# Kernel optimization log

Hardware: AMD Instinct MI355X
Metric: run time of the kernel (lower is better)

The kernel has to match this reference:

```python
import jax, jax.numpy as jnp
import numpy as np

FDIM, HDIM, DIM = 512, 512, 256
B, N = 64, 4096


def setup_inputs() -> dict:
    key = jax.random.key(0)
    k1, k2, k3, k4, k5 = jax.random.split(key, 5)
    image_features = jax.random.normal(k1, (B, N, FDIM), dtype=jnp.float32)
    hidden_state = jax.random.normal(k2, (B, HDIM), dtype=jnp.float32)
    # nn.Linear weights: stored [out, in]; y = x @ W.T
    W_img = jax.random.normal(k3, (DIM, FDIM), dtype=jnp.float32) * (FDIM ** -0.5)
    W_hid = jax.random.normal(k4, (DIM, HDIM), dtype=jnp.float32) * (HDIM ** -0.5)
    W_score = jax.random.normal(k5, (1, DIM), dtype=jnp.float32) * (DIM ** -0.5)
    return {"image_features": image_features, "hidden_state": hidden_state,
            "W_img": W_img, "W_hid": W_hid, "W_score": W_score}


def reference(image_features, hidden_state, W_img, W_hid, W_score):
    # proj_image: [B, N, D]
    proj_image = jnp.einsum('bnf,df->bnd', image_features, W_img)
    # proj_hidden: [B, 1, D]
    proj_hidden = jnp.einsum('bh,dh->bd', hidden_state, W_hid)[:, None, :]
    combined = jnp.tanh(proj_image + proj_hidden)            # [B, N, D]
    scores = jnp.einsum('bnd,d->bn', combined, W_score[0])   # [B, N]
    weights = jax.nn.softmax(scores, axis=-1)                # [B, N]
    context = jnp.einsum('bn,bnf->bf', weights, image_features)  # [B, F]
    return (context, weights)
```

## Files before the change

### kernel.cpp

```cpp
#include <hip/hip_runtime.h>
#include <hip/hip_bf16.h>

#define B_ 64
#define N_ 4096
#define F_ 512
#define D_ 256
#define BM 64
#define BK 64
#define APAD 520

typedef __attribute__((ext_vector_type(8))) short short8;
typedef __attribute__((ext_vector_type(4))) float f32x4;

__device__ __forceinline__ unsigned short f2bf(float f) {
  unsigned int u = __float_as_uint(f);
  u += 0x7FFFu + ((u >> 16) & 1u);
  return (unsigned short)(u >> 16);
}

__device__ __forceinline__ float fast_tanh(float x) {
  float e = __expf(-2.0f * fabsf(x));
  float t = (1.0f - e) / (1.0f + e);
  return copysignf(t, x);
}

__global__ void prep_w_kernel(const float* __restrict__ Wimg,
                              unsigned short* __restrict__ wfrag) {
  int d = blockIdx.x;
  int f = threadIdx.x;
  int kt = f >> 6, ks = (f >> 5) & 1, lg = (f >> 3) & 3, e = f & 7;
  int lr = d & 15, d16 = d >> 4;
  int lane = lg * 16 + lr;
  int idx = (((kt * 2 + ks) * 16 + d16) * 64 + lane) * 8 + e;
  wfrag[idx] = f2bf(Wimg[d * F_ + f]);
}

__global__ void prep_ph_kernel(const float* __restrict__ hid,
                               const float* __restrict__ Whid,
                               float* __restrict__ ph) {
  int b = blockIdx.x, d = threadIdx.x;
  const float4* hv = (const float4*)(hid + b * F_);
  const float4* wv = (const float4*)(Whid + d * F_);
  float acc = 0.f;
#pragma unroll 4
  for (int i = 0; i < 128; i++) {
    float4 h = hv[i], w = wv[i];
    acc += h.x * w.x + h.y * w.y + h.z * w.z + h.w * w.w;
  }
  ph[b * D_ + d] = acc;
}

__global__ __launch_bounds__(256, 2) void fused_kernel(
    const float* __restrict__ feat, const unsigned short* __restrict__ wfrag,
    const float* __restrict__ ph, const float* __restrict__ wscore,
    float* __restrict__ expw, float2* __restrict__ meta,
    float* __restrict__ part) {
  __shared__ unsigned short Afull[BM * APAD];
  __shared__ float red[BM][4];
  __shared__ float sbuf[BM];
  __shared__ float ewf[BM];

  int tid = threadIdx.x;
  int lane = tid & 63, wn = tid >> 6;
  int lr = lane & 15, lg = lane >> 4;

  int blk = blockIdx.x;
  int b = blk >> 6, chunk = blk & 63;
  int n0 = chunk * BM;

  const float* arow = feat + (size_t)(b * N_ + n0) * F_;

  f32x4 acc[4][4];
#pragma unroll
  for (int m = 0; m < 4; m++)
#pragma unroll
    for (int n = 0; n < 4; n++) acc[m][n] = (f32x4)0.f;

  int r_[4], c4_[4];
#pragma unroll
  for (int i = 0; i < 4; i++) {
    int idx4 = tid + i * 256;
    r_[i] = idx4 >> 4;
    c4_[i] = idx4 & 15;
  }

  float4 av[4];
#pragma unroll
  for (int i = 0; i < 4; i++)
    av[i] = *(const float4*)(arow + (size_t)r_[i] * F_ + c4_[i] * 4);
#pragma unroll
  for (int i = 0; i < 4; i++) {
    unsigned int p0 = (unsigned)f2bf(av[i].x) | ((unsigned)f2bf(av[i].y) << 16);
    unsigned int p1 = (unsigned)f2bf(av[i].z) | ((unsigned)f2bf(av[i].w) << 16);
    *(uint2*)(Afull + r_[i] * APAD + c4_[i] * 4) = make_uint2(p0, p1);
  }
  __syncthreads();

  for (int kt = 0; kt < F_ / BK; kt++) {
    if (kt < 7) {
#pragma unroll
      for (int i = 0; i < 4; i++)
        av[i] = *(const float4*)(arow + (size_t)r_[i] * F_ + (kt + 1) * BK + c4_[i] * 4);
    }
    short8 bfr[2][4], af[2][4];
#pragma unroll
    for (int ks = 0; ks < 2; ks++)
#pragma unroll
      for (int n = 0; n < 4; n++)
        bfr[ks][n] = *(const short8*)(wfrag +
            (size_t)(((kt * 2 + ks) * 16 + wn * 4 + n) * 64 + lane) * 8);
#pragma unroll
    for (int ks = 0; ks < 2; ks++)
#pragma unroll
      for (int m = 0; m < 4; m++)
        af[ks][m] = *(const short8*)(Afull + (m * 16 + lr) * APAD + kt * BK + ks * 32 + lg * 8);
#pragma unroll
    for (int ks = 0; ks < 2; ks++)
#pragma unroll
      for (int m = 0; m < 4; m++)
#pragma unroll
        for (int n = 0; n < 4; n++)
          acc[m][n] = __builtin_amdgcn_mfma_f32_16x16x32_bf16(af[ks][m], bfr[ks][n], acc[m][n], 0, 0, 0);
    if (kt < 7) {
#pragma unroll
      for (int i = 0; i < 4; i++) {
        unsigned int p0 = (unsigned)f2bf(av[i].x) | ((unsigned)f2bf(av[i].y) << 16);
        unsigned int p1 = (unsigned)f2bf(av[i].z) | ((unsigned)f2bf(av[i].w) << 16);
        *(uint2*)(Afull + r_[i] * APAD + (kt + 1) * BK + c4_[i] * 4) = make_uint2(p0, p1);
      }
    }
    __syncthreads();
  }

  float ph4[4], wv4[4];
#pragma unroll
  for (int n = 0; n < 4; n++) {
    int d = wn * 64 + n * 16 + lr;
    ph4[n] = ph[b * D_ + d];
    wv4[n] = wscore[d];
  }
#pragma unroll
  for (int m = 0; m < 4; m++) {
#pragma unroll
    for (int j = 0; j < 4; j++) {
      float p = 0.f;
#pragma unroll
      for (int n = 0; n < 4; n++)
        p += fast_tanh(acc[m][n][j] + ph4[n]) * wv4[n];
      p += __shfl_xor(p, 1);
      p += __shfl_xor(p, 2);
      p += __shfl_xor(p, 4);
      p += __shfl_xor(p, 8);
      if (lr == 0) red[m * 16 + lg * 4 + j][wn] = p;
    }
  }
  __syncthreads();
  if (tid < BM) sbuf[tid] = red[tid][0] + red[tid][1] + red[tid][2] + red[tid][3];
  __syncthreads();

  float mb = -1e30f;
#pragma unroll
  for (int r = 0; r < BM; r++) mb = fmaxf(mb, sbuf[r]);
  if (tid < BM) {
    float e = __expf(sbuf[tid] - mb);
    ewf[tid] = e;
    expw[b * N_ + n0 + tid] = e;
    float l = e;
#pragma unroll
    for (int o = 1; o < 64; o <<= 1) l += __shfl_xor(l, o);
    if (tid == 0) meta[blk] = make_float2(mb, l);
  }
  __syncthreads();

  int f0 = tid * 2;
  float a0 = 0.f, a1 = 0.f;
#pragma unroll 8
  for (int r = 0; r < BM; r++) {
    float w = ewf[r];
    unsigned int v = *(const unsigned int*)(Afull + r * APAD + f0);
    a0 += w * __uint_as_float(v << 16);
    a1 += w * __uint_as_float(v & 0xffff0000u);
  }
  float2 o; o.x = a0; o.y = a1;
  *(float2*)(part + (size_t)blk * F_ + f0) = o;
}

__global__ void finalize_kernel(const float* __restrict__ part,
                                const float2* __restrict__ meta,
                                const float* __restrict__ expw,
                                float* __restrict__ ctx,
                                float* __restrict__ wout) {
  __shared__ float sm[64], sl[64], se[64];
  int b = blockIdx.x, t = threadIdx.x;
  if (t < 64) {
    float2 ml = meta[b * 64 + t];
    sm[t] = ml.x;
    sl[t] = ml.y;
  }
  __syncthreads();
  float M = -1e30f;
#pragma unroll
  for (int i = 0; i < 64; i++) M = fmaxf(M, sm[i]);
  float Z = 0.f;
#pragma unroll
  for (int i = 0; i < 64; i++) Z += sl[i] * __expf(sm[i] - M);
  if (t < 64) se[t] = __expf(sm[t] - M);
  __syncthreads();
  float invZ = 1.0f / Z;
  float acc = 0.f;
#pragma unroll 8
  for (int i = 0; i < 64; i++) acc += part[(size_t)(b * 64 + i) * F_ + t] * se[i];
  ctx[b * F_ + t] = acc * invZ;
#pragma unroll
  for (int k = 0; k < 8; k++) {
    int n = k * 512 + t;
    wout[b * N_ + n] = expw[b * N_ + n] * se[n >> 6] * invZ;
  }
}

extern "C" void kernel_launch(void* const* d_in, const int* in_sizes, int n_in,
                              void* d_out, int out_size, void* d_ws, size_t ws_size,
                              hipStream_t stream) {
  const float* feat   = (const float*)d_in[0];
  const float* hid    = (const float*)d_in[1];
  const float* Wimg   = (const float*)d_in[2];
  const float* Whid   = (const float*)d_in[3];
  const float* Wscore = (const float*)d_in[4];

  float* ctx  = (float*)d_out;
  float* wout = (float*)d_out + B_ * F_;

  unsigned short* wfrag = (unsigned short*)d_ws;
  float*  ph    = (float*)((char*)d_ws + 262144);
  float*  expw  = (float*)((char*)d_ws + 327680);
  float2* meta  = (float2*)((char*)d_ws + 1376256);
  float*  part  = (float*)((char*)d_ws + 1409024);

  prep_w_kernel<<<D_, F_, 0, stream>>>(Wimg, wfrag);
  prep_ph_kernel<<<B_, D_, 0, stream>>>(hid, Whid, ph);
  fused_kernel<<<(B_ * N_) / BM, 256, 0, stream>>>(feat, wfrag, ph, Wscore, expw, meta, part);
  finalize_kernel<<<B_, 512, 0, stream>>>(part, meta, expw, ctx, wout);
}
```

Before: 241.3 us.

## Halve row tile, raise occupancy, and double-buffer feature prefetch across K steps

Shrinks the per-block row tile from 64 to 32 rows, which halves the shared-memory tile and allows four blocks per CU instead of two. The chunk count per batch row doubles, and the finalize kernel and workspace offsets are adjusted to match. The K loop now keeps two register buffers of feature loads in flight, and float-to-bf16 packing uses the packed intrinsic. The aim is to hide global-load latency on this memory-bound fused pass. In exchange, each block reloads the weight fragments for half as many rows, so weight traffic through the cache doubles, and the partial-context workspace and finalize reduction also double.

New measurement: 212.8 us. 11.8% less time.

```diff
diff --git a/kernel.cpp b/kernel.cpp
--- a/kernel.cpp
+++ b/kernel.cpp
@@ -5,9 +5,11 @@
 #define N_ 4096
 #define F_ 512
 #define D_ 256
-#define BM 64
+#define BM 32
 #define BK 64
 #define APAD 520
+#define NCHUNK (N_ / BM)
+#define NBLK (B_ * NCHUNK)
 
 typedef __attribute__((ext_vector_type(8))) short short8;
 typedef __attribute__((ext_vector_type(4))) float f32x4;
@@ -16,6 +18,13 @@
   unsigned int u = __float_as_uint(f);
   u += 0x7FFFu + ((u >> 16) & 1u);
   return (unsigned short)(u >> 16);
+}
+
+__device__ __forceinline__ unsigned int pk2bf(float x, float y) {
+  float2 f; f.x = x; f.y = y;
+  __hip_bfloat162 h = __float22bfloat162_rn(f);
+  union { __hip_bfloat162 h2; unsigned int u; } cv; cv.h2 = h;
+  return cv.u;
 }
 
 __device__ __forceinline__ float fast_tanh(float x) {
@@ -50,7 +59,7 @@
   ph[b * D_ + d] = acc;
 }
 
-__global__ __launch_bounds__(256, 2) void fused_kernel(
+__global__ __launch_bounds__(256, 4) void fused_kernel(
     const float* __restrict__ feat, const unsigned short* __restrict__ wfrag,
     const float* __restrict__ ph, const float* __restrict__ wscore,
     float* __restrict__ expw, float2* __restrict__ meta,
@@ -65,70 +74,64 @@
   int lr = lane & 15, lg = lane >> 4;
 
   int blk = blockIdx.x;
-  int b = blk >> 6, chunk = blk & 63;
+  int b = blk >> 7, chunk = blk & 127;
   int n0 = chunk * BM;
 
   const float* arow = feat + (size_t)(b * N_ + n0) * F_;
 
-  f32x4 acc[4][4];
-#pragma unroll
-  for (int m = 0; m < 4; m++)
+  f32x4 acc[2][4];
+#pragma unroll
+  for (int m = 0; m < 2; m++)
 #pragma unroll
     for (int n = 0; n < 4; n++) acc[m][n] = (f32x4)0.f;
 
-  int r_[4], c4_[4];
-#pragma unroll
-  for (int i = 0; i < 4; i++) {
+  int r_[2], c4_[2];
+#pragma unroll
+  for (int i = 0; i < 2; i++) {
     int idx4 = tid + i * 256;
     r_[i] = idx4 >> 4;
     c4_[i] = idx4 & 15;
   }
 
-  float4 av[4];
-#pragma unroll
-  for (int i = 0; i < 4; i++)
-    av[i] = *(const float4*)(arow + (size_t)r_[i] * F_ + c4_[i] * 4);
-#pragma unroll
-  for (int i = 0; i < 4; i++) {
-    unsigned int p0 = (unsigned)f2bf(av[i].x) | ((unsigned)f2bf(av[i].y) << 16);
-    unsigned int p1 = (unsigned)f2bf(av[i].z) | ((unsigned)f2bf(av[i].w) << 16);
-    *(uint2*)(Afull + r_[i] * APAD + c4_[i] * 4) = make_uint2(p0, p1);
-  }
-  __syncthreads();
-
-  for (int kt = 0; kt < F_ / BK; kt++) {
-    if (kt < 7) {
-#pragma unroll
-      for (int i = 0; i < 4; i++)
-        av[i] = *(const float4*)(arow + (size_t)r_[i] * F_ + (kt + 1) * BK + c4_[i] * 4);
-    }
-    short8 bfr[2][4], af[2][4];
-#pragma unroll
-    for (int ks = 0; ks < 2; ks++)
-#pragma unroll
-      for (int n = 0; n < 4; n++)
-        bfr[ks][n] = *(const short8*)(wfrag +
-            (size_t)(((kt * 2 + ks) * 16 + wn * 4 + n) * 64 + lane) * 8);
-#pragma unroll
-    for (int ks = 0; ks < 2; ks++)
-#pragma unroll
-      for (int m = 0; m < 4; m++)
-        af[ks][m] = *(const short8*)(Afull + (m * 16 + lr) * APAD + kt * BK + ks * 32 + lg * 8);
-#pragma unroll
-    for (int ks = 0; ks < 2; ks++)
-#pragma unroll
-      for (int m = 0; m < 4; m++)
-#pragma unroll
-        for (int n = 0; n < 4; n++)
-          acc[m][n] = __builtin_amdgcn_mfma_f32_16x16x32_bf16(af[ks][m], bfr[ks][n], acc[m][n], 0, 0, 0);
-    if (kt < 7) {
-#pragma unroll
-      for (int i = 0; i < 4; i++) {
-        unsigned int p0 = (unsigned)f2bf(av[i].x) | ((unsigned)f2bf(av[i].y) << 16);
-        unsigned int p1 = (unsigned)f2bf(av[i].z) | ((unsigned)f2bf(av[i].w) << 16);
-        *(uint2*)(Afull + r_[i] * APAD + (kt + 1) * BK + c4_[i] * 4) = make_uint2(p0, p1);
-      }
-    }
+#define LOADA(buf, kt_)                                                        \
+  _Pragma("unroll") for (int i = 0; i < 2; i++)                                \
+      buf[i] = *(const float4*)(arow + (size_t)r_[i] * F_ + (kt_)*BK + c4_[i] * 4);
+
+#define CVTWRITE(buf, kt_)                                                     \
+  _Pragma("unroll") for (int i = 0; i < 2; i++) {                              \
+    unsigned int p0 = pk2bf(buf[i].x, buf[i].y);                               \
+    unsigned int p1 = pk2bf(buf[i].z, buf[i].w);                               \
+    *(uint2*)(Afull + r_[i] * APAD + (kt_)*BK + c4_[i] * 4) = make_uint2(p0, p1); \
+  }
+
+#define MFMASTEP(kt_)                                                          \
+  _Pragma("unroll") for (int ks = 0; ks < 2; ks++) {                           \
+    short8 bfr[4], af[2];                                                      \
+    _Pragma("unroll") for (int n = 0; n < 4; n++)                              \
+        bfr[n] = *(const short8*)(wfrag +                                      \
+            (size_t)((((kt_)*2 + ks) * 16 + wn * 4 + n) * 64 + lane) * 8);     \
+    _Pragma("unroll") for (int m = 0; m < 2; m++)                              \
+        af[m] = *(const short8*)(Afull + (m * 16 + lr) * APAD + (kt_)*BK + ks * 32 + lg * 8); \
+    _Pragma("unroll") for (int m = 0; m < 2; m++)                              \
+      _Pragma("unroll") for (int n = 0; n < 4; n++)                            \
+        acc[m][n] = __builtin_amdgcn_mfma_f32_16x16x32_bf16(af[m], bfr[n], acc[m][n], 0, 0, 0); \
+  }
+
+  float4 rA[2], rB[2];
+  LOADA(rA, 0);
+  LOADA(rB, 1);
+  CVTWRITE(rA, 0);
+  __syncthreads();
+
+#pragma unroll
+  for (int kt = 0; kt < 8; kt += 2) {
+    if (kt + 2 < 8) { LOADA(rA, kt + 2); }
+    MFMASTEP(kt);
+    CVTWRITE(rB, kt + 1);
+    __syncthreads();
+    if (kt + 3 < 8) { LOADA(rB, kt + 3); }
+    MFMASTEP(kt + 1);
+    if (kt + 2 < 8) { CVTWRITE(rA, kt + 2); }
     __syncthreads();
   }
 
@@ -140,7 +143,7 @@
     wv4[n] = wscore[d];
   }
 #pragma unroll
-  for (int m = 0; m < 4; m++) {
+  for (int m = 0; m < 2; m++) {
 #pragma unroll
     for (int j = 0; j < 4; j++) {
       float p = 0.f;
@@ -167,7 +170,7 @@
     expw[b * N_ + n0 + tid] = e;
     float l = e;
 #pragma unroll
-    for (int o = 1; o < 64; o <<= 1) l += __shfl_xor(l, o);
+    for (int o = 1; o < 32; o <<= 1) l += __shfl_xor(l, o);
     if (tid == 0) meta[blk] = make_float2(mb, l);
   }
   __syncthreads();
@@ -190,31 +193,31 @@
                                 const float* __restrict__ expw,
                                 float* __restrict__ ctx,
                                 float* __restrict__ wout) {
-  __shared__ float sm[64], sl[64], se[64];
+  __shared__ float sm[NCHUNK], sl[NCHUNK], se[NCHUNK];
   int b = blockIdx.x, t = threadIdx.x;
-  if (t < 64) {
-    float2 ml = meta[b * 64 + t];
+  if (t < NCHUNK) {
+    float2 ml = meta[b * NCHUNK + t];
     sm[t] = ml.x;
     sl[t] = ml.y;
   }
   __syncthreads();
   float M = -1e30f;
-#pragma unroll
-  for (int i = 0; i < 64; i++) M = fmaxf(M, sm[i]);
+#pragma unroll 8
+  for (int i = 0; i < NCHUNK; i++) M = fmaxf(M, sm[i]);
   float Z = 0.f;
-#pragma unroll
-  for (int i = 0; i < 64; i++) Z += sl[i] * __expf(sm[i] - M);
-  if (t < 64) se[t] = __expf(sm[t] - M);
+#pragma unroll 8
+  for (int i = 0; i < NCHUNK; i++) Z += sl[i] * __expf(sm[i] - M);
+  if (t < NCHUNK) se[t] = __expf(sm[t] - M);
   __syncthreads();
   float invZ = 1.0f / Z;
   float acc = 0.f;
 #pragma unroll 8
-  for (int i = 0; i < 64; i++) acc += part[(size_t)(b * 64 + i) * F_ + t] * se[i];
+  for (int i = 0; i < NCHUNK; i++) acc += part[(size_t)(b * NCHUNK + i) * F_ + t] * se[i];
   ctx[b * F_ + t] = acc * invZ;
 #pragma unroll
   for (int k = 0; k < 8; k++) {
     int n = k * 512 + t;
-    wout[b * N_ + n] = expw[b * N_ + n] * se[n >> 6] * invZ;
+    wout[b * N_ + n] = expw[b * N_ + n] * se[n >> 5] * invZ;
   }
 }
 
@@ -234,10 +237,10 @@
   float*  ph    = (float*)((char*)d_ws + 262144);
   float*  expw  = (float*)((char*)d_ws + 327680);
   float2* meta  = (float2*)((char*)d_ws + 1376256);
-  float*  part  = (float*)((char*)d_ws + 1409024);
+  float*  part  = (float*)((char*)d_ws + 1441792);
 
   prep_w_kernel<<<D_, F_, 0, stream>>>(Wimg, wfrag);
   prep_ph_kernel<<<B_, D_, 0, stream>>>(hid, Whid, ph);
-  fused_kernel<<<(B_ * N_) / BM, 256, 0, stream>>>(feat, wfrag, ph, Wscore, expw, meta, part);
+  fused_kernel<<<NBLK, 256, 0, stream>>>(feat, wfrag, ph, Wscore, expw, meta, part);
   finalize_kernel<<<B_, 512, 0, stream>>>(part, meta, expw, ctx, wout);
 }
```
